# Kernel tuning notes

Hardware: AMD Instinct MI355X
Metric: run time of the kernel (lower is better)

## Reference

```python
import jax, jax.numpy as jnp
import numpy as np

C_WEIGHT = 0.005  # 'c' hyperparameter

def _psi(v):
    return jnp.sign(v) * jnp.log1p(jnp.abs(v))

def setup_inputs() -> dict:
    key = jax.random.key(0)
    ks = jax.random.split(key, 16)
    B, P, C = 64, 128, 72
    s = lambda fan_in: 1.0 / np.sqrt(fan_in)
    return {
        'x': jax.random.normal(ks[0], (B, P, 4), dtype=jnp.float32),
        'h': jax.random.normal(ks[1], (B, P, C), dtype=jnp.float32),
        'We1': jax.random.normal(ks[2], (2 * C + 2, 72), dtype=jnp.float32) * s(2 * C + 2),
        'be1': jnp.zeros((72,), dtype=jnp.float32),
        'We2': jax.random.normal(ks[3], (72, 72), dtype=jnp.float32) * s(72),
        'be2': jnp.zeros((72,), dtype=jnp.float32),
        'Wm': jax.random.normal(ks[4], (72, 1), dtype=jnp.float32) * s(72),
        'bm': jnp.zeros((1,), dtype=jnp.float32),
        'Wh1': jax.random.normal(ks[5], (C + 72, 72), dtype=jnp.float32) * s(C + 72),
        'bh1': jnp.zeros((72,), dtype=jnp.float32),
        'Wh2': jax.random.normal(ks[6], (72, 72), dtype=jnp.float32) * s(72),
        'bh2': jnp.zeros((72,), dtype=jnp.float32),
        'Wx': jax.random.normal(ks[7], (72, 1), dtype=jnp.float32) * s(72),
    }

def reference(x, h, We1, be1, We2, be2, Wm, bm, Wh1, bh1, Wh2, bh2, Wx):
    B, P, _ = x.shape
    # pairwise Minkowski invariants: take(...,0)*2 - sum == t^2 - |vec|^2
    x1 = x[:, :, None, :]  # (B,P,1,4)
    x2 = x[:, None, :, :]  # (B,1,P,4)
    d2 = jnp.square(x1 - x2)                      # (B,P,P,4)
    norms = 2.0 * d2[..., 0] - d2.sum(axis=-1)    # (B,P,P)
    z = x1 * x2
    prods = 2.0 * z[..., 0] - z.sum(axis=-1)      # (B,P,P)
    norms = _psi(norms)[..., None]                # use_psi=True
    prods = _psi(prods)[..., None]
    H = h.shape[-1]
    h1 = jnp.broadcast_to(h[:, :, None, :], (B, P, P, H))
    h2 = jnp.broadcast_to(h[:, None, :, :], (B, P, P, H))
    feat = jnp.concatenate([h1, h2, norms, prods], axis=-1)  # (B,P,P,2H+2)
    # phi_e: two Dense+ReLU
    m = jax.nn.relu(feat @ We1 + be1)
    m = jax.nn.relu(m @ We2 + be2)                # (B,P,P,72)
    # phi_m: Dense(1) + sigmoid
    w = jax.nn.sigmoid(m @ Wm + bm)               # (B,P,P,1)
    wm = jnp.sum(w * m, axis=2)                   # (B,P,72)
    # phi_h: Dense+ReLU, Dense; residual add
    g = jax.nn.relu(jnp.concatenate([h, wm], axis=-1) @ Wh1 + bh1)
    dh = g @ Wh2 + bh2
    h_out = h + dh
    # phi_x: Dense(1, no bias); x update
    phi_x = m @ Wx                                # (B,P,P,1)
    x_out = x + C_WEIGHT * jnp.mean(phi_x * x[:, None, :, :], axis=2)
    return (h_out, x_out)
```

## Files before the change

### kernel.cpp

```cpp
#include <hip/hip_runtime.h>
#include <hip/hip_bf16.h>
#include <math.h>

#define B_ 64
#define P_ 128
#define C_ 72
#define PADC 80
#define IT 8

typedef __attribute__((ext_vector_type(8))) _Float16 half8v;
typedef __attribute__((ext_vector_type(4))) _Float16 half4v;
typedef __attribute__((ext_vector_type(4))) float f32x4;
typedef __attribute__((ext_vector_type(2))) float f32x2;

#define FRAG_WE2  0
#define FRAG_WE1A (15 * 64)
#define FRAG_WE1B (30 * 64)
#define FRAG_WH1  (45 * 64)
#define FRAG_WH2  (70 * 64)
#define NFRAG 85

__device__ __forceinline__ float psi_f(float v) {
    float a = fabsf(v);
    return copysignf(__logf(1.0f + a), v);
}
template <int CTRL>
__device__ __forceinline__ float dpp_add(float v) {
    int s = __builtin_amdgcn_update_dpp(0, __builtin_bit_cast(int, v), CTRL, 0xF, 0xF, true);
    return v + __builtin_bit_cast(float, s);
}
__device__ __forceinline__ float red16(float v) {
    v = dpp_add<0xB1>(v);
    v = dpp_add<0x4E>(v);
    v = dpp_add<0x141>(v);
    v = dpp_add<0x140>(v);
    return v;
}
__device__ __forceinline__ half8v cvt8(const float* p) {
    f32x4 a = *(const f32x4*)p;
    f32x4 b = *(const f32x4*)(p + 4);
    half8v r = {(_Float16)a[0], (_Float16)a[1], (_Float16)a[2], (_Float16)a[3],
                (_Float16)b[0], (_Float16)b[1], (_Float16)b[2], (_Float16)b[3]};
    return r;
}

__global__ __launch_bounds__(64) void setup_kernel(
    const float* __restrict__ We1, const float* __restrict__ be1,
    const float* __restrict__ We2, const float* __restrict__ be2,
    const float* __restrict__ Wh1, const float* __restrict__ bh1,
    const float* __restrict__ Wh2, const float* __restrict__ bh2,
    const float* __restrict__ Wm, const float* __restrict__ Wx,
    half8v* __restrict__ frags)
{
    const int bid = blockIdx.x;
    const int l = threadIdx.x;
    const int c16 = l & 15, g = l >> 4;

    if (bid == NFRAG + 5) {
        _Float16* w12p = (_Float16*)((half4v*)(frags + NFRAG * 64) + 5 * 64);
        for (int i = l; i < 160; i += 64) {
            int s = i / 80, c = i - s * 80;
            w12p[i] = (c < C_) ? (_Float16)We1[(144 + s) * C_ + c] : (_Float16)0.f;
        }
        f32x2* wmwxp = (f32x2*)(w12p + 160);
        for (int idx = l; idx < 80; idx += 64) {
            f32x2 v;
            v[0] = (idx < C_) ? Wm[idx] : 0.f;
            v[1] = (idx < C_) ? Wx[idx] : 0.f;
            wmwxp[idx] = v;
        }
        return;
    }
    if (bid >= NFRAG) {
        half4v* tail = (half4v*)(frags + NFRAG * 64);
        const int nt = bid - NFRAG;
        const int n = nt * 16 + c16;
        half4v f = {};
        if (n < C_) {
            #pragma unroll
            for (int jj = 0; jj < 4; ++jj) {
                int k = 64 + 4 * g + jj;
                float w = 0.f;
                if (k < C_) w = We2[k * C_ + n];
                else if (k == C_) w = be2[n];
                f[jj] = (_Float16)w;
            }
        }
        tail[nt * 64 + l] = f;
        return;
    }

    const float* W;
    const float* bias;
    int kmax, rel;
    if (bid < 15)      { W = We2;            bias = be2;     kmax = 72;  rel = bid; }
    else if (bid < 30) { W = We1;            bias = nullptr; kmax = 72;  rel = bid - 15; }
    else if (bid < 45) { W = We1 + 72 * C_;  bias = be1;     kmax = 72;  rel = bid - 30; }
    else if (bid < 70) { W = Wh1;            bias = bh1;     kmax = 144; rel = bid - 45; }
    else               { W = Wh2;            bias = bh2;     kmax = 72;  rel = bid - 70; }
    const int kt = rel / 5, nt = rel - 5 * kt;
    const int n = nt * 16 + c16;

    half8v f = {};
    if (n < C_) {
        #pragma unroll
        for (int jj = 0; jj < 8; ++jj) {
            int k = kt * 32 + g * 8 + jj;
            float w = 0.f;
            if (k < kmax) w = W[k * C_ + n];
            else if (k == kmax && bias) w = bias[n];
            f[jj] = (_Float16)w;
        }
    }
    frags[bid * 64 + l] = f;
}

__global__ __launch_bounds__(64) void pre_kernel(
    const float* __restrict__ h, const half8v* __restrict__ frags,
    _Float16* __restrict__ Ah, half8v* __restrict__ Bcf,
    half4v* __restrict__ Bcft)
{
    __shared__ _Float16 T[16][88];
    const int l = threadIdx.x, c16 = l & 15, g = l >> 4;
    const int sel = blockIdx.x & 1;
    const int m0 = (blockIdx.x >> 1) * 16;

    const float* hrow = h + (m0 + c16) * C_;
    half8v a0 = cvt8(hrow + g * 8);
    half8v a1 = cvt8(hrow + 32 + g * 8);
    half8v a2 = {};
    if (g == 0) a2 = cvt8(hrow + 64);
    else if (g == 1) a2[0] = (_Float16)1.0f;

    const half8v* F = frags + (sel ? FRAG_WE1B : FRAG_WE1A);
    f32x4 acc[5] = {};
    #pragma unroll
    for (int kt = 0; kt < 3; ++kt) {
        half8v a = (kt == 0) ? a0 : (kt == 1 ? a1 : a2);
        #pragma unroll
        for (int nt = 0; nt < 5; ++nt)
            acc[nt] = __builtin_amdgcn_mfma_f32_16x16x32_f16(a, F[(kt * 5 + nt) * 64 + l], acc[nt], 0, 0, 0);
    }

    if (sel == 0) {
        #pragma unroll
        for (int nt = 0; nt < 5; ++nt) {
            int n = nt * 16 + c16;
            if (n < C_) {
                #pragma unroll
                for (int r = 0; r < 4; ++r)
                    Ah[(m0 + 4 * g + r) * PADC + n] = (_Float16)acc[nt][r];
            }
        }
        if (l < 16) {
            half4v one = {(_Float16)1.0f, (_Float16)0.f, (_Float16)0.f, (_Float16)0.f};
            half4v z = {};
            *(half4v*)&Ah[(m0 + l) * PADC + 72] = one;
            *(half4v*)&Ah[(m0 + l) * PADC + 76] = z;
        }
    } else {
        #pragma unroll
        for (int nt = 0; nt < 5; ++nt) {
            int n = nt * 16 + c16;
            if (n < C_) {
                #pragma unroll
                for (int r = 0; r < 4; ++r)
                    T[4 * g + r][n] = (_Float16)acc[nt][r];
            }
        }
        {
            int zr = l >> 2, zc = 72 + (l & 3) * 4;
            half4v z = {};
            *(half4v*)&T[zr][zc] = z;
        }
        __syncthreads();
        const int bb = m0 >> 7, jt = (m0 >> 4) & 7;
        half8v f0 = *(const half8v*)&T[c16][g * 8];
        half8v f1 = *(const half8v*)&T[c16][32 + g * 8];
        half4v ft = *(const half4v*)&T[c16][64 + g * 4];
        Bcf[((bb * 8 + jt) * 2 + 0) * 64 + l] = f0;
        Bcf[((bb * 8 + jt) * 2 + 1) * 64 + l] = f1;
        Bcft[(bb * 8 + jt) * 64 + l] = ft;
    }
}

__global__ __launch_bounds__(256, 2) void edge_kernel(
    const float* __restrict__ x, const _Float16* __restrict__ Ah,
    const half8v* __restrict__ Bcf, const half4v* __restrict__ Bcft,
    const half8v* __restrict__ frags,
    const float* __restrict__ bm,
    float* __restrict__ wm_out, float* __restrict__ xacc_out)
{
    const int b  = blockIdx.x >> 4;
    const int it = blockIdx.x & 15;
    const int t  = threadIdx.x;
    const int wv = t >> 6;
    const int l  = t & 63;
    const int c16 = l & 15;
    const int g   = l >> 4;

    half8v Wf[2][5];
    #pragma unroll
    for (int kt = 0; kt < 2; ++kt)
        #pragma unroll
        for (int nt = 0; nt < 5; ++nt)
            Wf[kt][nt] = frags[FRAG_WE2 + (kt * 5 + nt) * 64 + l];
    half4v Wf2[5];
    const half4v* tail = (const half4v*)(frags + NFRAG * 64);
    #pragma unroll
    for (int nt = 0; nt < 5; ++nt)
        Wf2[nt] = tail[nt * 64 + l];

    const _Float16* w12p = (const _Float16*)(tail + 5 * 64);
    half8v w1a = *(const half8v*)&w12p[g * 8];
    half8v w1b = *(const half8v*)&w12p[32 + g * 8];
    half4v w1t = *(const half4v*)&w12p[64 + g * 4];
    half8v w2a = *(const half8v*)&w12p[80 + g * 8];
    half8v w2b = *(const half8v*)&w12p[80 + 32 + g * 8];
    half4v w2t = *(const half4v*)&w12p[80 + 64 + g * 4];

    const f32x2* wmwxp = (const f32x2*)(w12p + 160);
    f32x2 WmWx[5][4];
    #pragma unroll
    for (int nt = 0; nt < 5; ++nt) {
        f32x4 p0 = *(const f32x4*)&wmwxp[nt * 16 + 4 * g];
        f32x4 p1 = *(const f32x4*)&wmwxp[nt * 16 + 4 * g + 2];
        WmWx[nt][0][0] = p0[0]; WmWx[nt][0][1] = p0[1];
        WmWx[nt][1][0] = p0[2]; WmWx[nt][1][1] = p0[3];
        WmWx[nt][2][0] = p1[0]; WmWx[nt][2][1] = p1[1];
        WmWx[nt][3][0] = p1[2]; WmWx[nt][3][1] = p1[3];
    }
    const float bm0 = bm[0];
    const f32x4 zero4 = {0.f, 0.f, 0.f, 0.f};

    const half8v* Bb = Bcf + (size_t)(b * 8) * 2 * 64;
    const half4v* Bt = Bcft + (size_t)(b * 8) * 64;
    const float*  xb = x + b * P_ * 4;
    const int c16_4 = c16 << 2;

    #pragma unroll 1
    for (int ii = 0; ii < 2; ++ii) {
        const int i = it * IT + wv * 2 + ii;
        const int node_i = b * P_ + i;
        const f32x4 xi = *(const f32x4*)&x[node_i * 4];
        const _Float16* Arow = Ah + node_i * PADC;
        half8v a0 = *(const half8v*)&Arow[g * 8];
        half8v a1 = *(const half8v*)&Arow[32 + g * 8];
        half4v at = *(const half4v*)&Arow[64 + g * 4];

        half8v bc0 = Bb[l];
        half8v bc1 = Bb[64 + l];
        half4v bct = Bt[l];

        f32x4 wmacc[5] = {};
        f32x4 xacc = {0.f, 0.f, 0.f, 0.f};

        #pragma unroll 1
        for (int q = 0; q < 2; ++q) {
            f32x4 xjq = *(const f32x4*)&xb[(q * 64 + l) * 4];
            float d0 = xi[0] - xjq[0], d1 = xi[1] - xjq[1];
            float d2 = xi[2] - xjq[2], d3 = xi[3] - xjq[3];
            float nn = d0 * d0 - d1 * d1 - d2 * d2 - d3 * d3;
            float pp = xi[0] * xjq[0] - xi[1] * xjq[1] - xi[2] * xjq[2] - xi[3] * xjq[3];
            unsigned geo =
                (unsigned)__builtin_bit_cast(unsigned short, (_Float16)psi_f(nn)) |
                ((unsigned)__builtin_bit_cast(unsigned short, (_Float16)psi_f(pp)) << 16);
            int geo0 = __builtin_amdgcn_ds_bpermute(c16_4,       (int)geo);
            int geo1 = __builtin_amdgcn_ds_bpermute(c16_4 + 64,  (int)geo);
            int geo2 = __builtin_amdgcn_ds_bpermute(c16_4 + 128, (int)geo);
            int geo3 = __builtin_amdgcn_ds_bpermute(c16_4 + 192, (int)geo);

            #pragma unroll
            for (int s = 0; s < 4; ++s) {
                const int jt = q * 4 + s;
                const int njt = (jt + 1) & 7;
                half8v nbc0 = Bb[(njt * 2) * 64 + l];
                half8v nbc1 = Bb[(njt * 2 + 1) * 64 + l];
                half4v nbct = Bt[njt * 64 + l];
                f32x4 xjv = *(const f32x4*)&xb[(jt * 16 + c16) * 4];

                int geos = (s == 0) ? geo0 : (s == 1) ? geo1 : (s == 2) ? geo2 : geo3;
                _Float16 nh = __builtin_bit_cast(_Float16, (unsigned short)((unsigned)geos & 0xFFFFu));
                _Float16 ph = __builtin_bit_cast(_Float16, (unsigned short)((unsigned)geos >> 16));
                half8v n8 = {nh, nh, nh, nh, nh, nh, nh, nh};
                half8v p8 = {ph, ph, ph, ph, ph, ph, ph, ph};
                half4v n4 = {nh, nh, nh, nh};
                half4v p4 = {ph, ph, ph, ph};
                half8v zero8 = {};
                half4v zero4h = {};

                half8v v0 = a0 + bc0;
                v0 = __builtin_elementwise_fma(w1a, n8, v0);
                v0 = __builtin_elementwise_fma(w2a, p8, v0);
                half8v af0 = __builtin_elementwise_max(v0, zero8);
                half8v v1 = a1 + bc1;
                v1 = __builtin_elementwise_fma(w1b, n8, v1);
                v1 = __builtin_elementwise_fma(w2b, p8, v1);
                half8v af1 = __builtin_elementwise_max(v1, zero8);
                half4v vt = at + bct;
                vt = __builtin_elementwise_fma(w1t, n4, vt);
                vt = __builtin_elementwise_fma(w2t, p4, vt);
                half4v af2 = __builtin_elementwise_max(vt, zero4h);

                f32x4 acc[5] = {};
                #pragma unroll
                for (int nt = 0; nt < 5; ++nt)
                    acc[nt] = __builtin_amdgcn_mfma_f32_16x16x32_f16(Wf[0][nt], af0, acc[nt], 0, 0, 0);
                #pragma unroll
                for (int nt = 0; nt < 5; ++nt)
                    acc[nt] = __builtin_amdgcn_mfma_f32_16x16x32_f16(Wf[1][nt], af1, acc[nt], 0, 0, 0);
                #pragma unroll
                for (int nt = 0; nt < 5; ++nt)
                    acc[nt] = __builtin_amdgcn_mfma_f32_16x16x16f16(Wf2[nt], af2, acc[nt], 0, 0, 0);

                f32x2 wdA = {0.f, 0.f}, wdB = {0.f, 0.f};
                #pragma unroll
                for (int nt = 0; nt < 5; ++nt) {
                    f32x4 m2q = __builtin_elementwise_max(acc[nt], zero4);
                    acc[nt] = m2q;
                    f32x2 e0 = {m2q[0], m2q[0]};
                    f32x2 e1 = {m2q[1], m2q[1]};
                    f32x2 e2 = {m2q[2], m2q[2]};
                    f32x2 e3 = {m2q[3], m2q[3]};
                    wdA = __builtin_elementwise_fma(e0, WmWx[nt][0], wdA);
                    wdB = __builtin_elementwise_fma(e1, WmWx[nt][1], wdB);
                    wdA = __builtin_elementwise_fma(e2, WmWx[nt][2], wdA);
                    wdB = __builtin_elementwise_fma(e3, WmWx[nt][3], wdB);
                }
                f32x2 wdpd = wdA + wdB;
                {
                    f32x2 sx;
                    sx[0] = __shfl_xor(wdpd[0], 16, 64);
                    sx[1] = __shfl_xor(wdpd[1], 16, 64);
                    wdpd += sx;
                    sx[0] = __shfl_xor(wdpd[0], 32, 64);
                    sx[1] = __shfl_xor(wdpd[1], 32, 64);
                    wdpd += sx;
                }
                float w_ = __builtin_amdgcn_rcpf(1.f + __expf(-(wdpd[0] + bm0)));
                f32x4 w4 = {w_, w_, w_, w_};
                #pragma unroll
                for (int nt = 0; nt < 5; ++nt)
                    wmacc[nt] = __builtin_elementwise_fma(w4, acc[nt], wmacc[nt]);
                f32x4 pd4 = {wdpd[1], wdpd[1], wdpd[1], wdpd[1]};
                xacc = __builtin_elementwise_fma(pd4, xjv, xacc);

                bc0 = nbc0; bc1 = nbc1; bct = nbct;
            }
        }

        #pragma unroll
        for (int nt = 0; nt < 5; ++nt)
            #pragma unroll
            for (int r = 0; r < 4; ++r)
                wmacc[nt][r] = red16(wmacc[nt][r]);
        #pragma unroll
        for (int q = 0; q < 4; ++q) xacc[q] = red16(xacc[q]);

        if (c16 == 0) {
            #pragma unroll
            for (int nt = 0; nt < 5; ++nt)
                #pragma unroll
                for (int r = 0; r < 4; ++r) {
                    int ch = nt * 16 + 4 * g + r;
                    if (ch < C_) wm_out[node_i * C_ + ch] = wmacc[nt][r];
                }
        }
        if (l == 0)
            *(f32x4*)&xacc_out[node_i * 4] = xacc;
    }
}

__global__ __launch_bounds__(64) void node_kernel(
    const float* __restrict__ x, const float* __restrict__ h,
    const half8v* __restrict__ frags,
    const float* __restrict__ wm, const float* __restrict__ xacc,
    float* __restrict__ hout, float* __restrict__ xout)
{
    __shared__ _Float16 g_s[16][88];
    const int l = threadIdx.x, c16 = l & 15, g = l >> 4;
    const int m0 = blockIdx.x * 16;

    const float* hrow  = h  + (m0 + c16) * C_;
    const float* wmrow = wm + (m0 + c16) * C_;

    half8v a[5];
    #pragma unroll
    for (int kt = 0; kt < 5; ++kt) {
        int k = kt * 32 + g * 8;
        half8v v = {};
        if (k < C_) v = cvt8(hrow + k);
        else if (k < 144) v = cvt8(wmrow + (k - C_));
        else if (k == 144) v[0] = (_Float16)1.0f;
        a[kt] = v;
    }
    f32x4 acc1[5] = {};
    #pragma unroll
    for (int kt = 0; kt < 5; ++kt)
        #pragma unroll
        for (int nt = 0; nt < 5; ++nt)
            acc1[nt] = __builtin_amdgcn_mfma_f32_16x16x32_f16(
                a[kt], frags[FRAG_WH1 + (kt * 5 + nt) * 64 + l], acc1[nt], 0, 0, 0);

    #pragma unroll
    for (int nt = 0; nt < 5; ++nt) {
        int n = nt * 16 + c16;
        #pragma unroll
        for (int r = 0; r < 4; ++r)
            g_s[4 * g + r][n] = (_Float16)fmaxf(acc1[nt][r], 0.f);
    }
    __syncthreads();
    half8v b0 = *(const half8v*)&g_s[c16][g * 8];
    half8v b1 = *(const half8v*)&g_s[c16][32 + g * 8];
    half8v b2 = {};
    if (g == 0) b2 = *(const half8v*)&g_s[c16][64];
    else if (g == 1) b2[0] = (_Float16)1.0f;

    f32x4 acc2[5] = {};
    #pragma unroll
    for (int kt = 0; kt < 3; ++kt) {
        half8v aa = (kt == 0) ? b0 : (kt == 1 ? b1 : b2);
        #pragma unroll
        for (int nt = 0; nt < 5; ++nt)
            acc2[nt] = __builtin_amdgcn_mfma_f32_16x16x32_f16(
                aa, frags[FRAG_WH2 + (kt * 5 + nt) * 64 + l], acc2[nt], 0, 0, 0);
    }
    #pragma unroll
    for (int nt = 0; nt < 5; ++nt) {
        int n = nt * 16 + c16;
        if (n < C_) {
            #pragma unroll
            for (int r = 0; r < 4; ++r) {
                int row = m0 + 4 * g + r;
                hout[row * C_ + n] = h[row * C_ + n] + acc2[nt][r];
            }
        }
    }
    {
        int row = m0 + (l >> 2), d = l & 3;
        xout[row * 4 + d] = x[row * 4 + d] + 0.005f * (xacc[row * 4 + d] * (1.0f / 128.f));
    }
}

extern "C" void kernel_launch(void* const* d_in, const int* in_sizes, int n_in,
                              void* d_out, int out_size, void* d_ws, size_t ws_size,
                              hipStream_t stream) {
    const float* x   = (const float*)d_in[0];
    const float* h   = (const float*)d_in[1];
    const float* We1 = (const float*)d_in[2];
    const float* be1 = (const float*)d_in[3];
    const float* We2 = (const float*)d_in[4];
    const float* be2 = (const float*)d_in[5];
    const float* Wm  = (const float*)d_in[6];
    const float* bm  = (const float*)d_in[7];
    const float* Wh1 = (const float*)d_in[8];
    const float* bh1 = (const float*)d_in[9];
    const float* Wh2 = (const float*)d_in[10];
    const float* bh2 = (const float*)d_in[11];
    const float* Wx  = (const float*)d_in[12];

    const int NNODE = B_ * P_;
    _Float16* Ah  = (_Float16*)d_ws;
    half8v* Bcf   = (half8v*)(Ah + NNODE * PADC);
    half4v* Bcft  = (half4v*)(Bcf + B_ * 8 * 2 * 64);
    float* wm     = (float*)(Bcft + B_ * 8 * 64);
    float* xacc   = wm + NNODE * C_;
    half8v* frags = (half8v*)(xacc + NNODE * 4);

    float* hout = (float*)d_out;
    float* xout = hout + NNODE * C_;

    setup_kernel<<<NFRAG + 6, 64, 0, stream>>>(We1, be1, We2, be2, Wh1, bh1, Wh2, bh2,
                                               Wm, Wx, frags);
    pre_kernel<<<NNODE / 16 * 2, 64, 0, stream>>>(h, frags, Ah, Bcf, Bcft);
    edge_kernel<<<B_ * 16, 256, 0, stream>>>(x, Ah, Bcf, Bcft, frags, bm, wm, xacc);
    node_kernel<<<NNODE / 16, 64, 0, stream>>>(x, h, frags, wm, xacc, hout, xout);
}
```

Baseline: 54.45 us.

## Fuse node MLP into edge kernel via shared-memory wm tile

```diff
diff --git a/kernel.cpp b/kernel.cpp
--- a/kernel.cpp
+++ b/kernel.cpp
@@ -185,12 +185,16 @@
 }
 
 __global__ __launch_bounds__(256, 2) void edge_kernel(
-    const float* __restrict__ x, const _Float16* __restrict__ Ah,
+    const float* __restrict__ x, const float* __restrict__ h,
+    const _Float16* __restrict__ Ah,
     const half8v* __restrict__ Bcf, const half4v* __restrict__ Bcft,
     const half8v* __restrict__ frags,
     const float* __restrict__ bm,
-    float* __restrict__ wm_out, float* __restrict__ xacc_out)
+    float* __restrict__ hout, float* __restrict__ xout)
 {
+    __shared__ float wm_s[IT][80];
+    __shared__ _Float16 g_s[16][88];
+
     const int b  = blockIdx.x >> 4;
     const int it = blockIdx.x & 15;
     const int t  = threadIdx.x;
@@ -237,11 +241,12 @@
     const half4v* Bt = Bcft + (size_t)(b * 8) * 64;
     const float*  xb = x + b * P_ * 4;
     const int c16_4 = c16 << 2;
+    const int m0row = b * P_ + it * IT;
 
     #pragma unroll 1
     for (int ii = 0; ii < 2; ++ii) {
-        const int i = it * IT + wv * 2 + ii;
-        const int node_i = b * P_ + i;
+        const int rowl = wv * 2 + ii;
+        const int node_i = m0row + rowl;
         const f32x4 xi = *(const f32x4*)&x[node_i * 4];
         const _Float16* Arow = Ah + node_i * PADC;
         half8v a0 = *(const half8v*)&Arow[g * 8];
@@ -363,82 +368,75 @@
                 #pragma unroll
                 for (int r = 0; r < 4; ++r) {
                     int ch = nt * 16 + 4 * g + r;
-                    if (ch < C_) wm_out[node_i * C_ + ch] = wmacc[nt][r];
+                    if (ch < C_) wm_s[rowl][ch] = wmacc[nt][r];
                 }
         }
-        if (l == 0)
-            *(f32x4*)&xacc_out[node_i * 4] = xacc;
-    }
-}
-
-__global__ __launch_bounds__(64) void node_kernel(
-    const float* __restrict__ x, const float* __restrict__ h,
-    const half8v* __restrict__ frags,
-    const float* __restrict__ wm, const float* __restrict__ xacc,
-    float* __restrict__ hout, float* __restrict__ xout)
-{
-    __shared__ _Float16 g_s[16][88];
-    const int l = threadIdx.x, c16 = l & 15, g = l >> 4;
-    const int m0 = blockIdx.x * 16;
-
-    const float* hrow  = h  + (m0 + c16) * C_;
-    const float* wmrow = wm + (m0 + c16) * C_;
-
-    half8v a[5];
-    #pragma unroll
-    for (int kt = 0; kt < 5; ++kt) {
-        int k = kt * 32 + g * 8;
-        half8v v = {};
-        if (k < C_) v = cvt8(hrow + k);
-        else if (k < 144) v = cvt8(wmrow + (k - C_));
-        else if (k == 144) v[0] = (_Float16)1.0f;
-        a[kt] = v;
-    }
-    f32x4 acc1[5] = {};
-    #pragma unroll
-    for (int kt = 0; kt < 5; ++kt)
-        #pragma unroll
-        for (int nt = 0; nt < 5; ++nt)
-            acc1[nt] = __builtin_amdgcn_mfma_f32_16x16x32_f16(
-                a[kt], frags[FRAG_WH1 + (kt * 5 + nt) * 64 + l], acc1[nt], 0, 0, 0);
-
-    #pragma unroll
-    for (int nt = 0; nt < 5; ++nt) {
-        int n = nt * 16 + c16;
-        #pragma unroll
-        for (int r = 0; r < 4; ++r)
-            g_s[4 * g + r][n] = (_Float16)fmaxf(acc1[nt][r], 0.f);
-    }
+        if (l == 0) {
+            f32x4 xo = xi + 0.005f * (1.0f / 128.f) * xacc;
+            *(f32x4*)&xout[node_i * 4] = xo;
+        }
+    }
+
     __syncthreads();
-    half8v b0 = *(const half8v*)&g_s[c16][g * 8];
-    half8v b1 = *(const half8v*)&g_s[c16][32 + g * 8];
-    half8v b2 = {};
-    if (g == 0) b2 = *(const half8v*)&g_s[c16][64];
-    else if (g == 1) b2[0] = (_Float16)1.0f;
-
-    f32x4 acc2[5] = {};
-    #pragma unroll
-    for (int kt = 0; kt < 3; ++kt) {
-        half8v aa = (kt == 0) ? b0 : (kt == 1 ? b1 : b2);
-        #pragma unroll
-        for (int nt = 0; nt < 5; ++nt)
-            acc2[nt] = __builtin_amdgcn_mfma_f32_16x16x32_f16(
-                aa, frags[FRAG_WH2 + (kt * 5 + nt) * 64 + l], acc2[nt], 0, 0, 0);
-    }
-    #pragma unroll
-    for (int nt = 0; nt < 5; ++nt) {
-        int n = nt * 16 + c16;
-        if (n < C_) {
-            #pragma unroll
-            for (int r = 0; r < 4; ++r) {
-                int row = m0 + 4 * g + r;
-                hout[row * C_ + n] = h[row * C_ + n] + acc2[nt][r];
+
+    if (wv != 0) return;
+    {
+        const int row = c16 & 7;
+        const float* hrow = h + (m0row + row) * C_;
+
+        half8v a[5];
+        #pragma unroll
+        for (int kt = 0; kt < 5; ++kt) {
+            int k = kt * 32 + g * 8;
+            half8v v = {};
+            if (k < C_) v = cvt8(hrow + k);
+            else if (k < 144) v = cvt8(&wm_s[row][k - C_]);
+            else if (k == 144) v[0] = (_Float16)1.0f;
+            a[kt] = v;
+        }
+        f32x4 acc1[5] = {};
+        #pragma unroll
+        for (int kt = 0; kt < 5; ++kt)
+            #pragma unroll
+            for (int nt = 0; nt < 5; ++nt)
+                acc1[nt] = __builtin_amdgcn_mfma_f32_16x16x32_f16(
+                    a[kt], frags[FRAG_WH1 + (kt * 5 + nt) * 64 + l], acc1[nt], 0, 0, 0);
+
+        #pragma unroll
+        for (int nt = 0; nt < 5; ++nt) {
+            int n = nt * 16 + c16;
+            #pragma unroll
+            for (int r = 0; r < 4; ++r)
+                g_s[4 * g + r][n] = (_Float16)fmaxf(acc1[nt][r], 0.f);
+        }
+        half8v b0 = *(const half8v*)&g_s[c16][g * 8];
+        half8v b1 = *(const half8v*)&g_s[c16][32 + g * 8];
+        half8v b2 = {};
+        if (g == 0) b2 = *(const half8v*)&g_s[c16][64];
+        else if (g == 1) b2[0] = (_Float16)1.0f;
+
+        f32x4 acc2[5] = {};
+        #pragma unroll
+        for (int kt = 0; kt < 3; ++kt) {
+            half8v aa = (kt == 0) ? b0 : (kt == 1 ? b1 : b2);
+            #pragma unroll
+            for (int nt = 0; nt < 5; ++nt)
+                acc2[nt] = __builtin_amdgcn_mfma_f32_16x16x32_f16(
+                    aa, frags[FRAG_WH2 + (kt * 5 + nt) * 64 + l], acc2[nt], 0, 0, 0);
+        }
+        if (g < 2) {
+            #pragma unroll
+            for (int nt = 0; nt < 5; ++nt) {
+                int n = nt * 16 + c16;
+                if (n < C_) {
+                    #pragma unroll
+                    for (int r = 0; r < 4; ++r) {
+                        int rw = m0row + 4 * g + r;
+                        hout[rw * C_ + n] = h[rw * C_ + n] + acc2[nt][r];
+                    }
+                }
             }
         }
-    }
-    {
-        int row = m0 + (l >> 2), d = l & 3;
-        xout[row * 4 + d] = x[row * 4 + d] + 0.005f * (xacc[row * 4 + d] * (1.0f / 128.f));
     }
 }
 
@@ -463,9 +461,7 @@
     _Float16* Ah  = (_Float16*)d_ws;
     half8v* Bcf   = (half8v*)(Ah + NNODE * PADC);
     half4v* Bcft  = (half4v*)(Bcf + B_ * 8 * 2 * 64);
-    float* wm     = (float*)(Bcft + B_ * 8 * 64);
-    float* xacc   = wm + NNODE * C_;
-    half8v* frags = (half8v*)(xacc + NNODE * 4);
+    half8v* frags = (half8v*)(Bcft + B_ * 8 * 64);
 
     float* hout = (float*)d_out;
     float* xout = hout + NNODE * C_;
@@ -473,6 +469,5 @@
     setup_kernel<<<NFRAG + 6, 64, 0, stream>>>(We1, be1, We2, be2, Wh1, bh1, Wh2, bh2,
                                                Wm, Wx, frags);
     pre_kernel<<<NNODE / 16 * 2, 64, 0, stream>>>(h, frags, Ah, Bcf, Bcft);
-    edge_kernel<<<B_ * 16, 256, 0, stream>>>(x, Ah, Bcf, Bcft, frags, bm, wm, xacc);
-    node_kernel<<<NNODE / 16, 64, 0, stream>>>(x, h, frags, wm, xacc, hout, xout);
-}
+    edge_kernel<<<B_ * 16, 256, 0, stream>>>(x, h, Ah, Bcf, Bcft, frags, bm, hout, xout);
+}
```

After: 52.01 us. 4.5% less time.
